# Optimization experiments

Hardware: AMD Instinct MI355X
Metric: run time of the kernel (lower is better)

The kernel has to match this reference:

```python
import jax, jax.numpy as jnp
import numpy as np

N, E, G = 100000, 1600000, 64   # nodes, edges, graphs
IN, H, OUT = 32, 128, 3


def setup_inputs() -> dict:
    key = jax.random.key(0)
    ks = jax.random.split(key, 24)
    def w(k, i, o):
        return (jax.random.normal(k, (i, o), jnp.float32) / np.sqrt(i)).astype(jnp.float32)
    inp = {
        "x": jax.random.normal(ks[0], (N, IN), jnp.float32),
        "edge_index": jax.random.randint(ks[1], (2, E), 0, N, dtype=jnp.int32).astype(jnp.int64),
        "batch": jnp.sort(jax.random.randint(ks[2], (N,), 0, G, dtype=jnp.int32)).astype(jnp.int64),
        # SAGEConv layer 0 (in->hidden): lin_l (neighbors, with bias), lin_r (root, no bias)
        "Wl0": w(ks[3], IN, H), "bl0": jnp.zeros((H,), jnp.float32), "Wr0": w(ks[4], IN, H),
        # SAGEConv layers 1,2 (hidden->hidden)
        "Wl1": w(ks[5], H, H), "bl1": jnp.zeros((H,), jnp.float32), "Wr1": w(ks[6], H, H),
        "Wl2": w(ks[7], H, H), "bl2": jnp.zeros((H,), jnp.float32), "Wr2": w(ks[8], H, H),
        # output head
        "Wfc": w(ks[9], H, OUT), "bfc": jnp.zeros((OUT,), jnp.float32),
        # aux MLP on (dim1, dim3)
        "Wa1": w(ks[10], 2, H), "ba1": jnp.zeros((H,), jnp.float32),
        "Wa2": w(ks[11], H, H), "ba2": jnp.zeros((H,), jnp.float32),
        "Wao": w(ks[12], H, 1), "bao": jnp.zeros((1,), jnp.float32),
    }
    return inp


def _sage_conv(x, src, dst, Wl, bl, Wr):
    # PyG SAGEConv (mean aggr): out = lin_l(mean_{j in N(i)} x_j) + lin_r(x_i)
    msg = x[src]                                   # [E, d] gather
    agg = jax.ops.segment_sum(msg, dst, num_segments=N)
    cnt = jax.ops.segment_sum(jnp.ones((src.shape[0],), x.dtype), dst, num_segments=N)
    mean = agg / jnp.maximum(cnt, 1.0)[:, None]
    return mean @ Wl + bl + x @ Wr


def reference(x, edge_index, batch,
              Wl0, bl0, Wr0, Wl1, bl1, Wr1, Wl2, bl2, Wr2,
              Wfc, bfc, Wa1, ba1, Wa2, ba2, Wao, bao):
    src, dst = edge_index[0], edge_index[1]
    h = jax.nn.relu(_sage_conv(x, src, dst, Wl0, bl0, Wr0))   # dropout is identity in eval
    h = jax.nn.relu(_sage_conv(h, src, dst, Wl1, bl1, Wr1))
    h = jax.nn.relu(_sage_conv(h, src, dst, Wl2, bl2, Wr2))
    main = h @ Wfc + bfc                                      # [N, 3]
    dim1, dim3 = main[:, 0], main[:, 2]
    aux_in = jnp.stack([dim1, dim3], axis=-1)                 # [N, 2]
    a = jax.nn.relu(aux_in @ Wa1 + ba1)
    a = jax.nn.relu(a @ Wa2 + ba2)
    aux_out = (a @ Wao + bao)[:, 0]                           # [N]
    final = jnp.stack([dim1, aux_out, dim3], axis=-1)         # [N, 3]
    # global mean pool over graph ids
    s = jax.ops.segment_sum(final, batch, num_segments=G)
    c = jax.ops.segment_sum(jnp.ones((final.shape[0],), final.dtype), batch, num_segments=G)
    return s / jnp.maximum(c, 1.0)[:, None]                   # [G, 3]
```

## Files before the change

kernel.cpp:

```cpp
#include <hip/hip_runtime.h>

#define NR 256
#define PART_CH 16384
typedef unsigned short ushortT;
typedef __attribute__((ext_vector_type(8))) short short8;
typedef __attribute__((ext_vector_type(4))) float float4v;
typedef __attribute__((ext_vector_type(2))) float float2v;

__device__ __forceinline__ unsigned short f32_to_bf16_rne(float f) {
    unsigned u = __float_as_uint(f);
    unsigned r = (u + 0x7fffu + ((u >> 16) & 1u)) >> 16;
    return (unsigned short)r;
}

__device__ __forceinline__ unsigned char f32_to_fp8(float f) {
    return (unsigned char)(__builtin_amdgcn_cvt_pk_fp8_f32(f, f, 0, false) & 0xff);
}

__device__ __forceinline__ void accum8(float* acc, uint4 v) {
    unsigned u[4] = {v.x, v.y, v.z, v.w};
#pragma unroll
    for (int q = 0; q < 4; q++) {
        acc[2 * q]     += __uint_as_float(u[q] << 16);
        acc[2 * q + 1] += __uint_as_float(u[q] & 0xffff0000u);
    }
}

__device__ __forceinline__ void accum16_fp8(float* acc, uint4 v) {
    unsigned u[4] = {v.x, v.y, v.z, v.w};
#pragma unroll
    for (int q = 0; q < 4; q++) {
        float2v lo = __builtin_amdgcn_cvt_pk_f32_fp8(u[q], false);
        float2v hi = __builtin_amdgcn_cvt_pk_f32_fp8(u[q], true);
        acc[4 * q + 0] += lo.x;
        acc[4 * q + 1] += lo.y;
        acc[4 * q + 2] += hi.x;
        acc[4 * q + 3] += hi.y;
    }
}


__launch_bounds__(256)
__global__ void hist_pass(const int* __restrict__ dst, int* __restrict__ hist_blk, int E, int NB) {
    __shared__ int h[512];
    int t = threadIdx.x;
    for (int j = t; j < 512; j += 256) h[j] = 0;
    __syncthreads();
    int e0 = blockIdx.x * PART_CH;
    int e1 = min(e0 + PART_CH, E);
    for (int base = e0; base < e1; base += 2048) {
        int idx = base + t;
        int d[8];
        int cnt = 0;
#pragma unroll
        for (int u = 0; u < 8; u++) {
            int e = idx + u * 256;
            if (e < e1) d[cnt++] = dst[e];
        }
        for (int u = 0; u < cnt; u++) atomicAdd(&h[d[u] >> 8], 1);
    }
    __syncthreads();
    int* row = hist_blk + (size_t)blockIdx.x * NB;
    for (int j = t; j < NB; j += 256) row[j] = h[j];
}

__launch_bounds__(256)
__global__ void col_scan(const int* __restrict__ hist_blk, int* __restrict__ pbase,
                         int* __restrict__ btot, int NB, int NBLK) {
    int bucket = blockIdx.x * 256 + threadIdx.x;
    if (bucket >= NB) return;
    int run = 0;
    int b = 0;
    for (; b + 4 <= NBLK; b += 4) {
        int v0 = hist_blk[(size_t)(b + 0) * NB + bucket];
        int v1 = hist_blk[(size_t)(b + 1) * NB + bucket];
        int v2 = hist_blk[(size_t)(b + 2) * NB + bucket];
        int v3 = hist_blk[(size_t)(b + 3) * NB + bucket];
        pbase[(size_t)(b + 0) * NB + bucket] = run;
        pbase[(size_t)(b + 1) * NB + bucket] = run + v0;
        pbase[(size_t)(b + 2) * NB + bucket] = run + v0 + v1;
        pbase[(size_t)(b + 3) * NB + bucket] = run + v0 + v1 + v2;
        run += v0 + v1 + v2 + v3;
    }
    for (; b < NBLK; b++) {
        size_t idx = (size_t)b * NB + bucket;
        int v = hist_blk[idx];
        pbase[idx] = run;
        run += v;
    }
    btot[bucket] = run;
}

__launch_bounds__(512)
__global__ void bstart_scan(const int* __restrict__ btot, int* __restrict__ bstart, int NB, int E) {
    __shared__ int sh[512];
    int t = threadIdx.x;
    int tot = (t < NB) ? btot[t] : 0;
    sh[t] = tot;
    __syncthreads();
    for (int off = 1; off < 512; off <<= 1) {
        int add = (t >= off) ? sh[t - off] : 0;
        __syncthreads();
        sh[t] += add;
        __syncthreads();
    }
    if (t < NB) bstart[t] = sh[t] - tot;
    if (t == 0) bstart[NB] = E;
}

__launch_bounds__(256)
__global__ void partition_edges(const int* __restrict__ src, const int* __restrict__ dst,
                                const int* __restrict__ pbase, const int* __restrict__ bstart,
                                unsigned* __restrict__ packed, int E, int NB) {
    __shared__ int cur[512];
    int t = threadIdx.x, b = blockIdx.x;
    const int* prow = pbase + (size_t)b * NB;
    for (int j = t; j < NB; j += 256) cur[j] = prow[j] + bstart[j];
    __syncthreads();
    int e0 = b * PART_CH;
    int e1 = min(e0 + PART_CH, E);
    for (int base = e0; base < e1; base += 2048) {
        int idx = base + t;
        int d[8], s[8];
        int cnt = 0;
#pragma unroll
        for (int u = 0; u < 8; u++) {
            int e = idx + u * 256;
            if (e < e1) { d[cnt] = dst[e]; s[cnt] = src[e]; cnt++; }
        }
        for (int u = 0; u < cnt; u++) {
            int dd = d[u];
            int pos = atomicAdd(&cur[dd >> 8], 1);
            packed[pos] = (unsigned)s[u] | ((unsigned)(dd & (NR - 1)) << 17);
        }
    }
}

__launch_bounds__(256)
__global__ void bucket_sort(const unsigned* __restrict__ packed, const int* __restrict__ bstart,
                            int* __restrict__ row_start, int* __restrict__ srcs, int N) {
    __shared__ int cnt[NR];
    __shared__ int sc[NR];
    __shared__ int cur[NR];
    int b = blockIdx.x, t = threadIdx.x;
    int nb0 = b * NR;
    int nnode = min(NR, N - nb0);
    int lo = bstart[b], hi = bstart[b + 1];
    cnt[t] = 0;
    if (t + 256 < NR) cnt[t + 256] = 0;
    __syncthreads();
    for (int base = lo; base < hi; base += 2048) {
        int idx = base + t;
        unsigned pk[8];
        int c = 0;
#pragma unroll
        for (int u = 0; u < 8; u++) {
            int e = idx + u * 256;
            if (e < hi) pk[c++] = packed[e];
        }
        for (int u = 0; u < c; u++) atomicAdd(&cnt[pk[u] >> 17], 1);
    }
    __syncthreads();
    sc[t] = cnt[t];
    __syncthreads();
    for (int off = 1; off < NR; off <<= 1) {
        int add = (t >= off) ? sc[t - off] : 0;
        __syncthreads();
        sc[t] += add;
        __syncthreads();
    }
    if (t < nnode) {
        int s = lo + sc[t] - cnt[t];
        row_start[nb0 + t] = s;
        cur[t] = s;
    }
    if (t == 0 && nb0 + nnode == N) row_start[N] = hi;
    __syncthreads();
    for (int base = lo; base < hi; base += 2048) {
        int idx = base + t;
        unsigned pk[8];
        int c = 0;
#pragma unroll
        for (int u = 0; u < 8; u++) {
            int e = idx + u * 256;
            if (e < hi) pk[c++] = packed[e];
        }
        for (int u = 0; u < c; u++) {
            int pos = atomicAdd(&cur[pk[u] >> 17], 1);
            srcs[pos] = (int)(pk[u] & 0x1FFFFu);
        }
    }
}


__global__ void prep_fused(const float* __restrict__ x, ushortT* __restrict__ xbf, int n4,
                           const float* __restrict__ Wl0, const float* __restrict__ Wr0,
                           const float* __restrict__ Wl1, const float* __restrict__ Wr1,
                           const float* __restrict__ Wl2, const float* __restrict__ Wr2,
                           const float* __restrict__ Wa2,
                           ushortT* __restrict__ Wt0, ushortT* __restrict__ Wt1,
                           ushortT* __restrict__ Wt2, ushortT* __restrict__ Wa2t) {
    int tid0 = blockIdx.x * 256 + threadIdx.x;
    if (tid0 < n4) {
        float4 v = ((const float4*)x)[tid0];
        ushort4 o;
        o.x = f32_to_bf16_rne(v.x);
        o.y = f32_to_bf16_rne(v.y);
        o.z = f32_to_bf16_rne(v.z);
        o.w = f32_to_bf16_rne(v.w);
        ((ushort4*)xbf)[tid0] = o;
        return;
    }
    int tid = tid0 - n4;
    if (tid < 8192) {
        int col = tid >> 6, k = tid & 63;
        float v = (k < 32) ? Wl0[k * 128 + col] : Wr0[(k - 32) * 128 + col];
        Wt0[col * 64 + ((k + 8 * col) & 63)] = f32_to_bf16_rne(v);
    } else if (tid < 8192 + 32768) {
        int j = tid - 8192;
        int col = j >> 8, k = j & 255;
        float v = (k < 128) ? Wl1[k * 128 + col] : Wr1[(k - 128) * 128 + col];
        Wt1[col * 256 + ((k + 8 * col) & 255)] = f32_to_bf16_rne(v);
    } else if (tid < 8192 + 65536) {
        int j = tid - 8192 - 32768;
        int col = j >> 8, k = j & 255;
        float v = (k < 128) ? Wl2[k * 128 + col] : Wr2[(k - 128) * 128 + col];
        Wt2[col * 256 + ((k + 8 * col) & 255)] = f32_to_bf16_rne(v);
    } else if (tid < 8192 + 65536 + 16384) {
        int j = tid - 8192 - 65536;
        int col = j >> 7, k = j & 127;
        Wa2t[col * 128 + ((k + 8 * col) & 127)] = f32_to_bf16_rne(Wa2[k * 128 + col]);
    }
}


template <int CPN>
__launch_bounds__(256)
__global__ void aggregate_mean_bf16(const uint4* __restrict__ hin, ushortT* __restrict__ out,
                                    const int* __restrict__ srcs, const int* __restrict__ rs, int n) {
    constexpr int TPN = CPN / 2;
    int tid = blockIdx.x * 256 + threadIdx.x;
    if (tid >= n * TPN) return;
    int i = tid / TPN;
    int c = tid & (TPN - 1);
    int lo = rs[i], hi = rs[i + 1];
    float acc0[8], acc1[8];
#pragma unroll
    for (int q = 0; q < 8; q++) { acc0[q] = 0.f; acc1[q] = 0.f; }
    int e = lo;
    for (; e + 8 <= hi; e += 8) {
        int s[8];
#pragma unroll
        for (int u = 0; u < 8; u++) s[u] = srcs[e + u];
        uint4 va[8], vb[8];
#pragma unroll
        for (int u = 0; u < 8; u++) {
            va[u] = hin[(size_t)s[u] * CPN + c];
            vb[u] = hin[(size_t)s[u] * CPN + c + TPN];
        }
#pragma unroll
        for (int u = 0; u < 8; u++) { accum8(acc0, va[u]); accum8(acc1, vb[u]); }
    }
    for (; e < hi; ++e) {
        int s = srcs[e];
        accum8(acc0, hin[(size_t)s * CPN + c]);
        accum8(acc1, hin[(size_t)s * CPN + c + TPN]);
    }
    float inv = 1.0f / (float)max(hi - lo, 1);
    uint4 o0, o1;
    o0.x = (unsigned)f32_to_bf16_rne(acc0[0] * inv) | ((unsigned)f32_to_bf16_rne(acc0[1] * inv) << 16);
    o0.y = (unsigned)f32_to_bf16_rne(acc0[2] * inv) | ((unsigned)f32_to_bf16_rne(acc0[3] * inv) << 16);
    o0.z = (unsigned)f32_to_bf16_rne(acc0[4] * inv) | ((unsigned)f32_to_bf16_rne(acc0[5] * inv) << 16);
    o0.w = (unsigned)f32_to_bf16_rne(acc0[6] * inv) | ((unsigned)f32_to_bf16_rne(acc0[7] * inv) << 16);
    o1.x = (unsigned)f32_to_bf16_rne(acc1[0] * inv) | ((unsigned)f32_to_bf16_rne(acc1[1] * inv) << 16);
    o1.y = (unsigned)f32_to_bf16_rne(acc1[2] * inv) | ((unsigned)f32_to_bf16_rne(acc1[3] * inv) << 16);
    o1.z = (unsigned)f32_to_bf16_rne(acc1[4] * inv) | ((unsigned)f32_to_bf16_rne(acc1[5] * inv) << 16);
    o1.w = (unsigned)f32_to_bf16_rne(acc1[6] * inv) | ((unsigned)f32_to_bf16_rne(acc1[7] * inv) << 16);
    ((uint4*)out)[(size_t)i * CPN + c] = o0;
    ((uint4*)out)[(size_t)i * CPN + c + TPN] = o1;
}


__launch_bounds__(256)
__global__ void aggregate_mean_fp8(const uint4* __restrict__ hin, ushortT* __restrict__ out,
                                   const int* __restrict__ srcs, const int* __restrict__ rs, int n) {
    int tid = blockIdx.x * 256 + threadIdx.x;
    if (tid >= n * 8) return;
    int i = tid >> 3;
    int c = tid & 7;
    int lo = rs[i], hi = rs[i + 1];
    float acc[16];
#pragma unroll
    for (int q = 0; q < 16; q++) acc[q] = 0.f;
    int e = lo;
    for (; e + 8 <= hi; e += 8) {
        int s[8];
#pragma unroll
        for (int u = 0; u < 8; u++) s[u] = srcs[e + u];
        uint4 v[8];
#pragma unroll
        for (int u = 0; u < 8; u++) v[u] = hin[(size_t)s[u] * 8 + c];
#pragma unroll
        for (int u = 0; u < 8; u++) accum16_fp8(acc, v[u]);
    }
    for (; e + 4 <= hi; e += 4) {
        int s[4];
#pragma unroll
        for (int u = 0; u < 4; u++) s[u] = srcs[e + u];
        uint4 v[4];
#pragma unroll
        for (int u = 0; u < 4; u++) v[u] = hin[(size_t)s[u] * 8 + c];
#pragma unroll
        for (int u = 0; u < 4; u++) accum16_fp8(acc, v[u]);
    }
    for (; e < hi; ++e) accum16_fp8(acc, hin[(size_t)srcs[e] * 8 + c]);
    float inv = 1.0f / (float)max(hi - lo, 1);
    uint4 o0, o1;
    o0.x = (unsigned)f32_to_bf16_rne(acc[0] * inv)  | ((unsigned)f32_to_bf16_rne(acc[1] * inv) << 16);
    o0.y = (unsigned)f32_to_bf16_rne(acc[2] * inv)  | ((unsigned)f32_to_bf16_rne(acc[3] * inv) << 16);
    o0.z = (unsigned)f32_to_bf16_rne(acc[4] * inv)  | ((unsigned)f32_to_bf16_rne(acc[5] * inv) << 16);
    o0.w = (unsigned)f32_to_bf16_rne(acc[6] * inv)  | ((unsigned)f32_to_bf16_rne(acc[7] * inv) << 16);
    o1.x = (unsigned)f32_to_bf16_rne(acc[8] * inv)  | ((unsigned)f32_to_bf16_rne(acc[9] * inv) << 16);
    o1.y = (unsigned)f32_to_bf16_rne(acc[10] * inv) | ((unsigned)f32_to_bf16_rne(acc[11] * inv) << 16);
    o1.z = (unsigned)f32_to_bf16_rne(acc[12] * inv) | ((unsigned)f32_to_bf16_rne(acc[13] * inv) << 16);
    o1.w = (unsigned)f32_to_bf16_rne(acc[14] * inv) | ((unsigned)f32_to_bf16_rne(acc[15] * inv) << 16);
    ((uint4*)out)[(size_t)i * 16 + c * 2]     = o0;
    ((uint4*)out)[(size_t)i * 16 + c * 2 + 1] = o1;
}


template <int KH, bool OUT_BF16, bool OUT_FP8>
__launch_bounds__(256, 2)
__global__ void gemm_mfma(const ushortT* __restrict__ Am, const ushortT* __restrict__ Ah,
                          const ushortT* __restrict__ Wt, const float* __restrict__ bias,
                          float* __restrict__ outf, ushortT* __restrict__ outbf,
                          unsigned char* __restrict__ outf8, int n) {
    constexpr int KT = 2 * KH;
    __shared__ ushortT sW[128 * KT];
    int t = threadIdx.x;
    constexpr int TOT16 = 128 * KT * 2 / 16;
    {
        const uint4* Wg = (const uint4*)Wt;
        uint4* Ws = (uint4*)sW;
        for (int j = t; j < TOT16; j += 256) Ws[j] = Wg[j];
    }
    __syncthreads();
    int wv = t >> 6, lane = t & 63;
    int q = lane >> 4, cid = lane & 15;
    int rbase = blockIdx.x * 128 + wv * 32;
    int r0 = rbase + cid, r1 = r0 + 16;
    int r0c = min(r0, n - 1), r1c = min(r1, n - 1);
    float4v acc[2][8];
#pragma unroll
    for (int i = 0; i < 2; i++)
#pragma unroll
        for (int j = 0; j < 8; j++) acc[i][j] = (float4v){0.f, 0.f, 0.f, 0.f};
    int swz = q * 8 + 8 * cid;
#pragma unroll
    for (int ks = 0; ks < KT / 32; ++ks) {
        int kk = ks * 32;
        const ushortT* abase = (kk < KH) ? Am : Ah;
        int kc = (kk < KH) ? kk : kk - KH;
        short8 a0 = *(const short8*)(abase + (size_t)r0c * KH + kc + q * 8);
        short8 a1 = *(const short8*)(abase + (size_t)r1c * KH + kc + q * 8);
#pragma unroll
        for (int j = 0; j < 8; ++j) {
            int col = j * 16 + cid;
            int p = (kk + swz + j * 128) & (KT - 1);
            short8 b = *(const short8*)(sW + col * KT + p);
            acc[0][j] = __builtin_amdgcn_mfma_f32_16x16x32_bf16(a0, b, acc[0][j], 0, 0, 0);
            acc[1][j] = __builtin_amdgcn_mfma_f32_16x16x32_bf16(a1, b, acc[1][j], 0, 0, 0);
        }
    }
    float bo[8];
#pragma unroll
    for (int j = 0; j < 8; ++j) bo[j] = bias[j * 16 + cid];
#pragma unroll
    for (int i = 0; i < 2; ++i) {
#pragma unroll
        for (int rr = 0; rr < 4; ++rr) {
            int row = rbase + i * 16 + q * 4 + rr;
            if (row < n) {
#pragma unroll
                for (int j = 0; j < 8; ++j) {
                    int col = j * 16 + cid;
                    float v = fmaxf(acc[i][j][rr] + bo[j], 0.f);
                    if (OUT_BF16) outbf[(size_t)row * 128 + col] = f32_to_bf16_rne(v);
                    if (OUT_FP8)  outf8[(size_t)row * 128 + col] = f32_to_fp8(v);
                    if (!OUT_BF16 && !OUT_FP8) outf[(size_t)row * 128 + col] = v;
                }
            }
        }
    }
}


template <int KH>
__launch_bounds__(256, 2)
__global__ void gemm_mfma_fin(const ushortT* __restrict__ Am, const ushortT* __restrict__ Ah,
                              const ushortT* __restrict__ Wt, const float* __restrict__ bias,
                              const float* __restrict__ Wfc, const float* __restrict__ bfc,
                              float* __restrict__ fin, int n) {
    constexpr int KT = 2 * KH;
    __shared__ ushortT sW[128 * KT];
    int t = threadIdx.x;
    constexpr int TOT16 = 128 * KT * 2 / 16;
    {
        const uint4* Wg = (const uint4*)Wt;
        uint4* Ws = (uint4*)sW;
        for (int j = t; j < TOT16; j += 256) Ws[j] = Wg[j];
    }
    __syncthreads();
    int wv = t >> 6, lane = t & 63;
    int q = lane >> 4, cid = lane & 15;
    int rbase = blockIdx.x * 128 + wv * 32;
    int r0 = rbase + cid, r1 = r0 + 16;
    int r0c = min(r0, n - 1), r1c = min(r1, n - 1);
    float4v acc[2][8];
#pragma unroll
    for (int i = 0; i < 2; i++)
#pragma unroll
        for (int j = 0; j < 8; j++) acc[i][j] = (float4v){0.f, 0.f, 0.f, 0.f};
    int swz = q * 8 + 8 * cid;
#pragma unroll
    for (int ks = 0; ks < KT / 32; ++ks) {
        int kk = ks * 32;
        const ushortT* abase = (kk < KH) ? Am : Ah;
        int kc = (kk < KH) ? kk : kk - KH;
        short8 a0 = *(const short8*)(abase + (size_t)r0c * KH + kc + q * 8);
        short8 a1 = *(const short8*)(abase + (size_t)r1c * KH + kc + q * 8);
#pragma unroll
        for (int j = 0; j < 8; ++j) {
            int col = j * 16 + cid;
            int p = (kk + swz + j * 128) & (KT - 1);
            short8 b = *(const short8*)(sW + col * KT + p);
            acc[0][j] = __builtin_amdgcn_mfma_f32_16x16x32_bf16(a0, b, acc[0][j], 0, 0, 0);
            acc[1][j] = __builtin_amdgcn_mfma_f32_16x16x32_bf16(a1, b, acc[1][j], 0, 0, 0);
        }
    }
    float bo[8], w1[8], w3[8];
#pragma unroll
    for (int j = 0; j < 8; ++j) {
        int col = j * 16 + cid;
        bo[j] = bias[col];
        w1[j] = Wfc[col * 3 + 0];
        w3[j] = Wfc[col * 3 + 2];
    }
    float bfc0 = bfc[0], bfc2 = bfc[2];
#pragma unroll
    for (int i = 0; i < 2; ++i) {
#pragma unroll
        for (int rr = 0; rr < 4; ++rr) {
            float p1 = 0.f, p3 = 0.f;
#pragma unroll
            for (int j = 0; j < 8; ++j) {
                float v = fmaxf(acc[i][j][rr] + bo[j], 0.f);
                p1 += v * w1[j];
                p3 += v * w3[j];
            }
            p1 += __shfl_xor(p1, 1, 64); p3 += __shfl_xor(p3, 1, 64);
            p1 += __shfl_xor(p1, 2, 64); p3 += __shfl_xor(p3, 2, 64);
            p1 += __shfl_xor(p1, 4, 64); p3 += __shfl_xor(p3, 4, 64);
            p1 += __shfl_xor(p1, 8, 64); p3 += __shfl_xor(p3, 8, 64);
            int row = rbase + i * 16 + q * 4 + rr;
            if (cid == 0 && row < n) {
                fin[(size_t)row * 3 + 0] = p1 + bfc0;
                fin[(size_t)row * 3 + 2] = p3 + bfc2;
            }
        }
    }
}


__launch_bounds__(256, 4)
__global__ void head_mfma(const ushortT* __restrict__ Wa2t, const float* __restrict__ Wa1,
                          const float* __restrict__ ba1, const float* __restrict__ ba2,
                          const float* __restrict__ Wao, const float* __restrict__ bao,
                          float* __restrict__ fin, int n) {
    __shared__ ushortT sW[128 * 128];
    __shared__ float sD1[128], sD3[128];
    __shared__ float sWa1a[128], sWa1b[128], sBa1[128];
    int t = threadIdx.x;
    {
        const uint4* Wg = (const uint4*)Wa2t;
        uint4* Ws = (uint4*)sW;
        for (int j = t; j < 2048; j += 256) Ws[j] = Wg[j];
    }
    int rbase = blockIdx.x * 128;
    if (t < 128) {
        sWa1a[t] = Wa1[t];
        sWa1b[t] = Wa1[128 + t];
        sBa1[t] = ba1[t];
        int row = min(rbase + t, n - 1);
        sD1[t] = fin[(size_t)row * 3 + 0];
        sD3[t] = fin[(size_t)row * 3 + 2];
    }
    __syncthreads();
    int wv = t >> 6, lane = t & 63;
    int q = lane >> 4, cid = lane & 15;
    int rl0 = wv * 32 + cid, rl1 = rl0 + 16;
    float d1a = sD1[rl0], d3a = sD3[rl0];
    float d1b = sD1[rl1], d3b = sD3[rl1];
    float4v acc[2][8];
#pragma unroll
    for (int i = 0; i < 2; i++)
#pragma unroll
        for (int j = 0; j < 8; j++) acc[i][j] = (float4v){0.f, 0.f, 0.f, 0.f};
    int swz = q * 8 + 8 * cid;
#pragma unroll
    for (int ks = 0; ks < 4; ++ks) {
        int k0 = ks * 32 + q * 8;
        short8 a0, a1;
#pragma unroll
        for (int j = 0; j < 8; ++j) {
            int k = k0 + j;
            float w0 = sWa1a[k], w1 = sWa1b[k], bb = sBa1[k];
            float v0 = fmaxf(fmaf(d1a, w0, fmaf(d3a, w1, bb)), 0.f);
            float v1 = fmaxf(fmaf(d1b, w0, fmaf(d3b, w1, bb)), 0.f);
            a0[j] = (short)f32_to_bf16_rne(v0);
            a1[j] = (short)f32_to_bf16_rne(v1);
        }
        int p = (ks * 32 + swz) & 127;
#pragma unroll
        for (int j = 0; j < 8; ++j) {
            short8 b = *(const short8*)(sW + (j * 16 + cid) * 128 + p);
            acc[0][j] = __builtin_amdgcn_mfma_f32_16x16x32_bf16(a0, b, acc[0][j], 0, 0, 0);
            acc[1][j] = __builtin_amdgcn_mfma_f32_16x16x32_bf16(a1, b, acc[1][j], 0, 0, 0);
        }
    }
    float b2[8], wo[8];
#pragma unroll
    for (int j = 0; j < 8; ++j) {
        int col = j * 16 + cid;
        b2[j] = ba2[col];
        wo[j] = Wao[col];
    }
    float bao0 = bao[0];
#pragma unroll
    for (int i = 0; i < 2; ++i) {
#pragma unroll
        for (int rr = 0; rr < 4; ++rr) {
            float s = 0.f;
#pragma unroll
            for (int j = 0; j < 8; ++j) s += fmaxf(acc[i][j][rr] + b2[j], 0.f) * wo[j];
            s += __shfl_xor(s, 1, 64);
            s += __shfl_xor(s, 2, 64);
            s += __shfl_xor(s, 4, 64);
            s += __shfl_xor(s, 8, 64);
            int row = rbase + wv * 32 + i * 16 + q * 4 + rr;
            if (cid == 0 && row < n) fin[(size_t)row * 3 + 1] = s + bao0;
        }
    }
}


__global__ void pool_kernel(const float* __restrict__ fin, const int* __restrict__ batch,
                            float* __restrict__ out, int n) {
    int g = blockIdx.x, t = threadIdx.x;
    int lo = 0, hi = n;
    while (lo < hi) { int mid = (lo + hi) >> 1; if (batch[mid] < g) lo = mid + 1; else hi = mid; }
    int start = lo;
    lo = 0; hi = n;
    while (lo < hi) { int mid = (lo + hi) >> 1; if (batch[mid] < g + 1) lo = mid + 1; else hi = mid; }
    int end = lo;
    float s0 = 0.f, s1 = 0.f, s2 = 0.f;
    for (int i = start + t; i < end; i += 256) {
        s0 += fin[(size_t)i * 3 + 0];
        s1 += fin[(size_t)i * 3 + 1];
        s2 += fin[(size_t)i * 3 + 2];
    }
    __shared__ float r0[256], r1[256], r2[256];
    r0[t] = s0; r1[t] = s1; r2[t] = s2;
    __syncthreads();
    for (int off = 128; off > 0; off >>= 1) {
        if (t < off) { r0[t] += r0[t + off]; r1[t] += r1[t + off]; r2[t] += r2[t + off]; }
        __syncthreads();
    }
    if (t == 0) {
        float c = (float)max(end - start, 1);
        out[g * 3 + 0] = r0[0] / c;
        out[g * 3 + 1] = r1[0] / c;
        out[g * 3 + 2] = r2[0] / c;
    }
}


extern "C" void kernel_launch(void* const* d_in, const int* in_sizes, int n_in,
                              void* d_out, int out_size, void* d_ws, size_t ws_size,
                              hipStream_t stream) {
    const float* x    = (const float*)d_in[0];
    const int*   ei   = (const int*)d_in[1];
    const int*   batch= (const int*)d_in[2];
    const float* Wl0  = (const float*)d_in[3];
    const float* bl0  = (const float*)d_in[4];
    const float* Wr0  = (const float*)d_in[5];
    const float* Wl1  = (const float*)d_in[6];
    const float* bl1  = (const float*)d_in[7];
    const float* Wr1  = (const float*)d_in[8];
    const float* Wl2  = (const float*)d_in[9];
    const float* bl2  = (const float*)d_in[10];
    const float* Wr2  = (const float*)d_in[11];
    const float* Wfc  = (const float*)d_in[12];
    const float* bfc  = (const float*)d_in[13];
    const float* Wa1  = (const float*)d_in[14];
    const float* ba1  = (const float*)d_in[15];
    const float* Wa2  = (const float*)d_in[16];
    const float* ba2  = (const float*)d_in[17];
    const float* Wao  = (const float*)d_in[18];
    const float* bao  = (const float*)d_in[19];

    const int N = in_sizes[0] / 32;
    const int E = in_sizes[1] / 2;
    const int G = out_size / 3;
    const int* src = ei;
    const int* dst = ei + E;
    float* out = (float*)d_out;
    const int NB = (N + NR - 1) / NR;
    const int NBLK = (E + PART_CH - 1) / PART_CH;

    char* p = (char*)d_ws;
    auto carve = [&](size_t bytes) {
        void* r = (void*)p;
        p += (bytes + 255) & ~(size_t)255;
        return r;
    };
    int*           hist_blk = (int*)carve((size_t)NBLK * NB * 4);
    int*           pbase    = (int*)carve((size_t)NBLK * NB * 4);
    int*           btot     = (int*)carve((size_t)NB * 4);
    int*           bstart   = (int*)carve((size_t)(NB + 1) * 4);
    int*           row_start= (int*)carve((size_t)(N + 1) * 4);
    unsigned*      packed   = (unsigned*)carve((size_t)E * 4);
    int*           srcs     = (int*)carve((size_t)E * 4);
    ushortT*       aggbf    = (ushortT*)carve((size_t)N * 128 * 2);
    ushortT*       xbf      = (ushortT*)carve((size_t)N * 32 * 2);
    ushortT*       hbf0     = (ushortT*)carve((size_t)N * 128 * 2);
    ushortT*       hbf1     = (ushortT*)carve((size_t)N * 128 * 2);
    unsigned char* hf8_0    = (unsigned char*)carve((size_t)N * 128);
    unsigned char* hf8_1    = (unsigned char*)carve((size_t)N * 128);
    float*         fin      = (float*)carve((size_t)N * 3 * 4);
    ushortT*       Wt0      = (ushortT*)carve((size_t)128 * 64 * 2);
    ushortT*       Wt1      = (ushortT*)carve((size_t)128 * 256 * 2);
    ushortT*       Wt2      = (ushortT*)carve((size_t)128 * 256 * 2);
    ushortT*       Wa2t     = (ushortT*)carve((size_t)128 * 128 * 2);

    const int gemm_grid = (N + 127) / 128;
    const int n4 = N * 32 / 4;

    prep_fused<<<(n4 + 90112 + 255) / 256, 256, 0, stream>>>(
        x, xbf, n4, Wl0, Wr0, Wl1, Wr1, Wl2, Wr2, Wa2, Wt0, Wt1, Wt2, Wa2t);

    hist_pass<<<NBLK, 256, 0, stream>>>(dst, hist_blk, E, NB);
    col_scan<<<(NB + 255) / 256, 256, 0, stream>>>(hist_blk, pbase, btot, NB, NBLK);
    bstart_scan<<<1, 512, 0, stream>>>(btot, bstart, NB, E);
    partition_edges<<<NBLK, 256, 0, stream>>>(src, dst, pbase, bstart, packed, E, NB);
    bucket_sort<<<NB, 256, 0, stream>>>(packed, bstart, row_start, srcs, N);

    aggregate_mean_bf16<4><<<(N * 2 + 255) / 256, 256, 0, stream>>>(
        (const uint4*)xbf, aggbf, srcs, row_start, N);
    gemm_mfma<32, true, true><<<gemm_grid, 256, 0, stream>>>(
        aggbf, xbf, Wt0, bl0, (float*)nullptr, hbf0, hf8_0, N);
    aggregate_mean_fp8<<<(N * 8 + 255) / 256, 256, 0, stream>>>(
        (const uint4*)hf8_0, aggbf, srcs, row_start, N);
    gemm_mfma<128, true, true><<<gemm_grid, 256, 0, stream>>>(
        aggbf, hbf0, Wt1, bl1, (float*)nullptr, hbf1, hf8_1, N);
    aggregate_mean_fp8<<<(N * 8 + 255) / 256, 256, 0, stream>>>(
        (const uint4*)hf8_1, aggbf, srcs, row_start, N);
    gemm_mfma_fin<128><<<gemm_grid, 256, 0, stream>>>(
        aggbf, hbf1, Wt2, bl2, Wfc, bfc, fin, N);

    head_mfma<<<gemm_grid, 256, 0, stream>>>(
        Wa2t, Wa1, ba1, ba2, Wao, bao, fin, N);

    pool_kernel<<<G, 256, 0, stream>>>(fin, batch, out, N);
}
```

Measured before the change: 376.3 us.

## Replace per-block histogram column scan with global atomic bucket counters

Graph CSR construction now keeps one global count per bucket, filled by atomics, in place of a per-block histogram matrix and its column scan. Partitioning re-counts each chunk locally and reserves space with an atomicAdd on a global cursor per bucket. Bucket size drops to 128 nodes and chunk size to 4096 edges, giving more partition blocks and more sort blocks. The aim is to remove the column-scan kernel and its matrix traffic and to use more blocks in parallel. In exchange, partition_edges reads dst twice, and the edge order inside a bucket is no longer deterministic.

```diff
diff --git a/kernel.cpp b/kernel.cpp
--- a/kernel.cpp
+++ b/kernel.cpp
@@ -1,7 +1,7 @@
 #include <hip/hip_runtime.h>
 
-#define NR 256
-#define PART_CH 16384
+#define NR 128
+#define PART_CH 4096
 typedef unsigned short ushortT;
 typedef __attribute__((ext_vector_type(8))) short short8;
 typedef __attribute__((ext_vector_type(4))) float float4v;
@@ -41,10 +41,10 @@
 
 
 __launch_bounds__(256)
-__global__ void hist_pass(const int* __restrict__ dst, int* __restrict__ hist_blk, int E, int NB) {
-    __shared__ int h[512];
+__global__ void bucket_count(const int* __restrict__ dst, int* __restrict__ bcnt, int E, int NB) {
+    __shared__ int h[1024];
     int t = threadIdx.x;
-    for (int j = t; j < 512; j += 256) h[j] = 0;
+    for (int j = t; j < NB; j += 256) h[j] = 0;
     __syncthreads();
     int e0 = blockIdx.x * PART_CH;
     int e1 = min(e0 + PART_CH, E);
@@ -57,70 +57,78 @@
             int e = idx + u * 256;
             if (e < e1) d[cnt++] = dst[e];
         }
-        for (int u = 0; u < cnt; u++) atomicAdd(&h[d[u] >> 8], 1);
-    }
-    __syncthreads();
-    int* row = hist_blk + (size_t)blockIdx.x * NB;
-    for (int j = t; j < NB; j += 256) row[j] = h[j];
+        for (int u = 0; u < cnt; u++) atomicAdd(&h[d[u] >> 7], 1);
+    }
+    __syncthreads();
+    for (int j = t; j < NB; j += 256) {
+        int v = h[j];
+        if (v) atomicAdd(&bcnt[j], v);
+    }
 }
 
 __launch_bounds__(256)
-__global__ void col_scan(const int* __restrict__ hist_blk, int* __restrict__ pbase,
-                         int* __restrict__ btot, int NB, int NBLK) {
-    int bucket = blockIdx.x * 256 + threadIdx.x;
-    if (bucket >= NB) return;
-    int run = 0;
-    int b = 0;
-    for (; b + 4 <= NBLK; b += 4) {
-        int v0 = hist_blk[(size_t)(b + 0) * NB + bucket];
-        int v1 = hist_blk[(size_t)(b + 1) * NB + bucket];
-        int v2 = hist_blk[(size_t)(b + 2) * NB + bucket];
-        int v3 = hist_blk[(size_t)(b + 3) * NB + bucket];
-        pbase[(size_t)(b + 0) * NB + bucket] = run;
-        pbase[(size_t)(b + 1) * NB + bucket] = run + v0;
-        pbase[(size_t)(b + 2) * NB + bucket] = run + v0 + v1;
-        pbase[(size_t)(b + 3) * NB + bucket] = run + v0 + v1 + v2;
-        run += v0 + v1 + v2 + v3;
-    }
-    for (; b < NBLK; b++) {
-        size_t idx = (size_t)b * NB + bucket;
-        int v = hist_blk[idx];
-        pbase[idx] = run;
-        run += v;
-    }
-    btot[bucket] = run;
-}
-
-__launch_bounds__(512)
-__global__ void bstart_scan(const int* __restrict__ btot, int* __restrict__ bstart, int NB, int E) {
-    __shared__ int sh[512];
+__global__ void bucket_scan(const int* __restrict__ bcnt, int* __restrict__ bstart,
+                            int* __restrict__ gcur, int NB, int E) {
+    __shared__ int sh[256];
     int t = threadIdx.x;
-    int tot = (t < NB) ? btot[t] : 0;
+    int v[4];
+    int tot = 0;
+#pragma unroll
+    for (int j = 0; j < 4; j++) {
+        int idx = t * 4 + j;
+        v[j] = (idx < NB) ? bcnt[idx] : 0;
+        tot += v[j];
+    }
     sh[t] = tot;
     __syncthreads();
-    for (int off = 1; off < 512; off <<= 1) {
+    for (int off = 1; off < 256; off <<= 1) {
         int add = (t >= off) ? sh[t - off] : 0;
         __syncthreads();
         sh[t] += add;
         __syncthreads();
     }
-    if (t < NB) bstart[t] = sh[t] - tot;
+    int run = sh[t] - tot;
+#pragma unroll
+    for (int j = 0; j < 4; j++) {
+        int idx = t * 4 + j;
+        if (idx < NB) { bstart[idx] = run; gcur[idx] = run; }
+        run += v[j];
+    }
     if (t == 0) bstart[NB] = E;
 }
 
 __launch_bounds__(256)
 __global__ void partition_edges(const int* __restrict__ src, const int* __restrict__ dst,
-                                const int* __restrict__ pbase, const int* __restrict__ bstart,
-                                unsigned* __restrict__ packed, int E, int NB) {
-    __shared__ int cur[512];
-    int t = threadIdx.x, b = blockIdx.x;
-    const int* prow = pbase + (size_t)b * NB;
-    for (int j = t; j < NB; j += 256) cur[j] = prow[j] + bstart[j];
-    __syncthreads();
-    int e0 = b * PART_CH;
+                                int* __restrict__ gcur, unsigned* __restrict__ packed,
+                                int E, int NB) {
+    __shared__ int hist[1024];
+    __shared__ int base[1024];
+    int t = threadIdx.x;
+    int e0 = blockIdx.x * PART_CH;
     int e1 = min(e0 + PART_CH, E);
-    for (int base = e0; base < e1; base += 2048) {
-        int idx = base + t;
+    for (int j = t; j < NB; j += 256) hist[j] = 0;
+    __syncthreads();
+    for (int bb = e0; bb < e1; bb += 2048) {
+        int idx = bb + t;
+        int d[8];
+        int cnt = 0;
+#pragma unroll
+        for (int u = 0; u < 8; u++) {
+            int e = idx + u * 256;
+            if (e < e1) d[cnt++] = dst[e];
+        }
+        for (int u = 0; u < cnt; u++) atomicAdd(&hist[d[u] >> 7], 1);
+    }
+    __syncthreads();
+    for (int j = t; j < NB; j += 256) {
+        int h = hist[j];
+        base[j] = h ? atomicAdd(&gcur[j], h) : 0;
+    }
+    __syncthreads();
+    for (int j = t; j < NB; j += 256) hist[j] = base[j];
+    __syncthreads();
+    for (int bb = e0; bb < e1; bb += 2048) {
+        int idx = bb + t;
         int d[8], s[8];
         int cnt = 0;
 #pragma unroll
@@ -130,7 +138,7 @@
         }
         for (int u = 0; u < cnt; u++) {
             int dd = d[u];
-            int pos = atomicAdd(&cur[dd >> 8], 1);
+            int pos = atomicAdd(&hist[dd >> 7], 1);
             packed[pos] = (unsigned)s[u] | ((unsigned)(dd & (NR - 1)) << 17);
         }
     }
@@ -146,11 +154,10 @@
     int nb0 = b * NR;
     int nnode = min(NR, N - nb0);
     int lo = bstart[b], hi = bstart[b + 1];
-    cnt[t] = 0;
-    if (t + 256 < NR) cnt[t + 256] = 0;
-    __syncthreads();
-    for (int base = lo; base < hi; base += 2048) {
-        int idx = base + t;
+    if (t < NR) cnt[t] = 0;
+    __syncthreads();
+    for (int bb = lo; bb < hi; bb += 2048) {
+        int idx = bb + t;
         unsigned pk[8];
         int c = 0;
 #pragma unroll
@@ -161,12 +168,12 @@
         for (int u = 0; u < c; u++) atomicAdd(&cnt[pk[u] >> 17], 1);
     }
     __syncthreads();
-    sc[t] = cnt[t];
+    if (t < NR) sc[t] = cnt[t];
     __syncthreads();
     for (int off = 1; off < NR; off <<= 1) {
-        int add = (t >= off) ? sc[t - off] : 0;
+        int add = (t >= off && t < NR) ? sc[t - off] : 0;
         __syncthreads();
-        sc[t] += add;
+        if (t < NR) sc[t] += add;
         __syncthreads();
     }
     if (t < nnode) {
@@ -176,8 +183,8 @@
     }
     if (t == 0 && nb0 + nnode == N) row_start[N] = hi;
     __syncthreads();
-    for (int base = lo; base < hi; base += 2048) {
-        int idx = base + t;
+    for (int bb = lo; bb < hi; bb += 2048) {
+        int idx = bb + t;
         unsigned pk[8];
         int c = 0;
 #pragma unroll
@@ -616,7 +623,6 @@
     const int* dst = ei + E;
     float* out = (float*)d_out;
     const int NB = (N + NR - 1) / NR;
-    const int NBLK = (E + PART_CH - 1) / PART_CH;
 
     char* p = (char*)d_ws;
     auto carve = [&](size_t bytes) {
@@ -624,10 +630,9 @@
         p += (bytes + 255) & ~(size_t)255;
         return r;
     };
-    int*           hist_blk = (int*)carve((size_t)NBLK * NB * 4);
-    int*           pbase    = (int*)carve((size_t)NBLK * NB * 4);
-    int*           btot     = (int*)carve((size_t)NB * 4);
+    int*           bcnt     = (int*)carve((size_t)NB * 4);
     int*           bstart   = (int*)carve((size_t)(NB + 1) * 4);
+    int*           gcur     = (int*)carve((size_t)NB * 4);
     int*           row_start= (int*)carve((size_t)(N + 1) * 4);
     unsigned*      packed   = (unsigned*)carve((size_t)E * 4);
     int*           srcs     = (int*)carve((size_t)E * 4);
@@ -644,15 +649,16 @@
     ushortT*       Wa2t     = (ushortT*)carve((size_t)128 * 128 * 2);
 
     const int gemm_grid = (N + 127) / 128;
+    const int part_grid = (E + PART_CH - 1) / PART_CH;
     const int n4 = N * 32 / 4;
 
     prep_fused<<<(n4 + 90112 + 255) / 256, 256, 0, stream>>>(
         x, xbf, n4, Wl0, Wr0, Wl1, Wr1, Wl2, Wr2, Wa2, Wt0, Wt1, Wt2, Wa2t);
 
-    hist_pass<<<NBLK, 256, 0, stream>>>(dst, hist_blk, E, NB);
-    col_scan<<<(NB + 255) / 256, 256, 0, stream>>>(hist_blk, pbase, btot, NB, NBLK);
-    bstart_scan<<<1, 512, 0, stream>>>(btot, bstart, NB, E);
-    partition_edges<<<NBLK, 256, 0, stream>>>(src, dst, pbase, bstart, packed, E, NB);
+    hipMemsetAsync(bcnt, 0, (size_t)NB * 4, stream);
+    bucket_count<<<part_grid, 256, 0, stream>>>(dst, bcnt, E, NB);
+    bucket_scan<<<1, 256, 0, stream>>>(bcnt, bstart, gcur, NB, E);
+    partition_edges<<<part_grid, 256, 0, stream>>>(src, dst, gcur, packed, E, NB);
     bucket_sort<<<NB, 256, 0, stream>>>(packed, bstart, row_start, srcs, N);
 
     aggregate_mean_bf16<4><<<(N * 2 + 255) / 256, 256, 0, stream>>>(
```

Result: faster. 358.0 us, median of 2 (-4.9%).
